# Kernel optimization log

Measured on AMD Instinct MI355X. Metric: run time of the kernel, lower is better.

The kernel has to match this reference:

```python
import jax, jax.numpy as jnp
import numpy as np

N, C_IN, HF, WF = 4, 256, 128, 128
IMG_H, IMG_W = 1024, 1024
A = 3  # anchors per location (1 size x 3 aspect ratios), matches RPNHead
OBJ_THR, IOU_THR = 0.3, 0.7
PRE_NMS, POST_NMS = 2000, 300  # pre-NMS top-k (== top_k_proposals_training), post-NMS top-k (testing)


def setup_inputs() -> dict:
    key = jax.random.key(0)
    ks = jax.random.split(key, 5)
    return {
        "feat": jax.random.normal(ks[0], (N, C_IN, HF, WF), jnp.float32),
        "conv_w": jax.random.normal(ks[1], (256, C_IN, 3, 3), jnp.float32) * 0.02,
        "conv_b": jnp.zeros((256,), jnp.float32),
        "det_w": jax.random.normal(ks[2], (A, 256, 1, 1), jnp.float32) * 0.05,
        "det_b": jnp.zeros((A,), jnp.float32),
        "reg_w": jax.random.normal(ks[3], (4 * A, 256, 1, 1), jnp.float32) * 0.02,
        "reg_b": jnp.zeros((4 * A,), jnp.float32),
    }


def _conv(x, w, b, pad):
    y = jax.lax.conv_general_dilated(x, w, (1, 1), [(pad, pad), (pad, pad)],
                                     dimension_numbers=("NCHW", "OIHW", "NCHW"))
    return y + b[None, :, None, None]


def _anchors():
    # AnchorGenerator.generate_anchors + grid_anchors, stride = image // grid
    scales = jnp.array([128.0], jnp.float32)
    ratios = jnp.array([0.5, 1.0, 2.0], jnp.float32)
    hr = jnp.sqrt(ratios)
    wr = 1.0 / hr
    ws = (wr[:, None] * scales[None, :]).reshape(-1)
    hs = (hr[:, None] * scales[None, :]).reshape(-1)
    base = jnp.round(jnp.stack([-ws, -hs, ws, hs], axis=1) / 2.0)  # [A,4]
    sx = jnp.arange(WF, dtype=jnp.float32) * (IMG_W // WF)
    sy = jnp.arange(HF, dtype=jnp.float32) * (IMG_H // HF)
    yy, xx = jnp.meshgrid(sy, sx, indexing="ij")
    shifts = jnp.stack([xx.ravel(), yy.ravel(), xx.ravel(), yy.ravel()], axis=1)  # [H*W,4]
    return (shifts[:, None, :] + base[None, :, :]).reshape(-1, 4)  # [H*W*A,4]


def _decode(anchors, deltas):
    # Faithful to source, including the x/y swap in the anchor-center computation.
    x1, y1, x2, y2 = anchors[..., 0], anchors[..., 1], anchors[..., 2], anchors[..., 3]
    aw = x2 - x1
    ah = y2 - y1
    acx = y1 + aw / 2  # (sic) matches original code
    acy = x1 + ah / 2  # (sic)
    dx, dy, dw, dh = deltas[..., 0], deltas[..., 1], deltas[..., 2], deltas[..., 3]
    px = acx + dx * aw
    py = acy + dy * ah
    pw = aw * jnp.exp(dw)
    ph = ah * jnp.exp(dh)
    return jnp.stack([px - pw / 2, py - ph / 2, px + pw / 2, py + ph / 2], axis=-1)


def _filter_one(boxes, scores):
    # clip -> degenerate filter -> objectness threshold -> NMS -> top-k, fixed shapes
    w = boxes[:, 2] - boxes[:, 0]
    h = boxes[:, 3] - boxes[:, 1]
    valid = (scores > OBJ_THR) & (w > 0) & (h > 0)
    s = jnp.where(valid, scores, -jnp.inf)
    top_s, top_i = jax.lax.top_k(s, PRE_NMS)
    b = boxes[top_i]
    v = valid[top_i]
    area = jnp.maximum(b[:, 2] - b[:, 0], 0) * jnp.maximum(b[:, 3] - b[:, 1], 0)
    ix1 = jnp.maximum(b[:, None, 0], b[None, :, 0])
    iy1 = jnp.maximum(b[:, None, 1], b[None, :, 1])
    ix2 = jnp.minimum(b[:, None, 2], b[None, :, 2])
    iy2 = jnp.minimum(b[:, None, 3], b[None, :, 3])
    inter = jnp.maximum(ix2 - ix1, 0) * jnp.maximum(iy2 - iy1, 0)
    iou = inter / jnp.maximum(area[:, None] + area[None, :] - inter, 1e-9)
    idxs = jnp.arange(PRE_NMS)

    def body(keep, i):
        sup = jnp.any((iou[i] > IOU_THR) & keep & (idxs < i))
        return keep.at[i].set(v[i] & ~sup), None

    keep, _ = jax.lax.scan(body, jnp.zeros(PRE_NMS, bool), idxs)
    fs = jnp.where(keep, top_s, -jnp.inf)
    sel_s, sel_i = jax.lax.top_k(fs, POST_NMS)
    kept = keep[sel_i]
    out = jnp.concatenate([b[sel_i], sel_s[:, None]], axis=-1)  # [POST,5] = box + score
    return jnp.where(kept[:, None], out, 0.0)


def reference(feat, conv_w, conv_b, det_w, det_b, reg_w, reg_b):
    x = _conv(feat, conv_w, conv_b, 1)                      # fpn conv 3x3, no activation
    obj = jax.nn.sigmoid(_conv(x, det_w, det_b, 0)).reshape(N, -1)  # [N, A*H*W]
    d = _conv(x, reg_w, reg_b, 0)                           # [N, 4A, H, W]
    d = d.reshape(N, 4, A, HF, WF).transpose(0, 2, 3, 4, 1).reshape(N, -1, 4)
    anchors = _anchors()                                    # [A_total, 4]
    props = _decode(anchors[None], d)
    props = jnp.stack([
        jnp.clip(props[..., 0], 0, IMG_W), jnp.clip(props[..., 1], 0, IMG_H),
        jnp.clip(props[..., 2], 0, IMG_W), jnp.clip(props[..., 3], 0, IMG_H)], axis=-1)
    return jax.vmap(_filter_one)(props, obj)  # [N, POST_NMS, 5]
```

## Files before the change

### kernel.cpp

```cpp
#include <hip/hip_runtime.h>
#include <hip/hip_bf16.h>
#include <hip/hip_fp16.h>
#include <stdint.h>
#include <math.h>

#define N_IMG 4
#define CIN 256
#define HFD 128
#define WFD 128
#define HW (HFD*WFD)
#define NA 3
#define NPROP (NA*HW)
#define PRE_NMS 2000
#define POST_NMS 300

__device__ __forceinline__ unsigned long long rl64(unsigned long long v, int i) {
    unsigned int lo = (unsigned int)__builtin_amdgcn_readlane((int)(unsigned int)v, i);
    unsigned int hi = (unsigned int)__builtin_amdgcn_readlane((int)(unsigned int)(v >> 32), i);
    return ((unsigned long long)hi << 32) | (unsigned long long)lo;
}

__device__ __forceinline__ double sum4(const double* __restrict__ PART, size_t cp) {
    const size_t S = (size_t)1 << 20;
    return (PART[cp] + PART[cp + S]) + (PART[cp + 2 * S] + PART[cp + 3 * S]);
}

__device__ __forceinline__ void decode_box(int i, double dx, double dy, double dwv, double dhv,
                                           double& c1o, double& c2o, double& c3o, double& c4o) {
    int loc = i / 3, aa = i % 3;
    int hh = loc >> 7, wwi = loc & 127;
    double sx = (double)(wwi * 8), sy = (double)(hh * 8);
    double bx1 = (aa == 0) ? -91.0 : (aa == 1 ? -64.0 : -45.0);
    double by1 = (aa == 0) ? -45.0 : (aa == 1 ? -64.0 : -91.0);
    double x1 = sx + bx1, y1 = sy + by1, x2 = sx - bx1, y2 = sy - by1;
    double aw = x2 - x1, ahh = y2 - y1;
    double acx = y1 + aw * 0.5;
    double acy = x1 + ahh * 0.5;
    double px = acx + dx * aw, py = acy + dy * ahh;
    double pw = aw * exp(dwv), ph = ahh * exp(dhv);
    double c1 = px - pw * 0.5, c2 = py - ph * 0.5, c3 = px + pw * 0.5, c4 = py + ph * 0.5;
    c1o = fmin(fmax(c1, 0.0), 1024.0);
    c2o = fmin(fmax(c2, 0.0), 1024.0);
    c3o = fmin(fmax(c3, 0.0), 1024.0);
    c4o = fmin(fmax(c4, 0.0), 1024.0);
}

__global__ __launch_bounds__(256) void k_effw64(const float* __restrict__ cw, const float* __restrict__ cb,
                                                const float* __restrict__ dw_, const float* __restrict__ db_,
                                                const float* __restrict__ rw_, const float* __restrict__ rb_,
                                                double* __restrict__ E64, double* __restrict__ EB64,
                                                unsigned long long* __restrict__ PSPREF,
                                                int* __restrict__ PSNEED,
                                                uint32_t* __restrict__ HIST,
                                                uint32_t* __restrict__ CNT)
{
    int b = blockIdx.x;
    int tid = threadIdx.x;
    if (b < 144) {
        __shared__ float hwl[15][260];
        __shared__ float wt[256][16];
        int k0 = b * 16;
        for (int idx = tid; idx < 15 * 256; idx += 256) {
            int c = idx >> 8, co = idx & 255;
            hwl[c][co] = (c < 3) ? dw_[c * 256 + co] : rw_[(c - 3) * 256 + co];
        }
        for (int idx = tid; idx < 4096; idx += 256) {
            int co = idx >> 4, kk = idx & 15;
            wt[co][kk] = cw[co * 2304 + k0 + kk];
        }
        __syncthreads();
        int kk = tid >> 4, c = tid & 15;
        double s = 0.0;
        if (c < 15) {
#pragma unroll 4
            for (int co = 0; co < 256; co++) s += (double)hwl[c][co] * (double)wt[co][kk];
        }
        E64[(k0 + kk) * 16 + c] = s;
    } else {
        if (tid < 16) {
            int c = tid;
            double s = 0.0; double hb = 0.0;
            if (c < 15) {
                const float* hw = (c < 3) ? (dw_ + c * 256) : (rw_ + (c - 3) * 256);
                for (int co = 0; co < 256; co++) s += (double)hw[co] * (double)cb[co];
                hb = (double)((c < 3) ? db_[c] : rb_[c - 3]);
            }
            EB64[c] = s + hb;
        }
        for (int i = tid; i < N_IMG * 2048; i += 256) HIST[i] = 0u;
        if (tid < N_IMG) { PSPREF[tid] = 0ull; PSNEED[tid] = PRE_NMS; CNT[tid] = 0u; }
    }
}

__global__ __launch_bounds__(256, 4) void k_conv64(const float* __restrict__ feat,
                                                   const double* __restrict__ E64,
                                                   double* __restrict__ PART)
{
    __shared__ float in_t[8][4][132];
    __shared__ double wl[8][9][16];
    int b = blockIdx.x;
    int chunk = b & 3; int hp = (b >> 2) & 63; int n = b >> 8;
    int h0 = hp * 2;
    int tid = threadIdx.x;
    int q = tid & 63;
    int row = q >> 5, qq = q & 31, w0 = qq * 4;
    int g = tid >> 6;
    double acc[4][4];
#pragma unroll
    for (int cc = 0; cc < 4; cc++)
#pragma unroll
        for (int px = 0; px < 4; px++) acc[cc][px] = 0.0;

    for (int sl = 0; sl < 8; sl++) {
        int ci0 = (chunk << 6) + sl * 8;
        for (int t = tid; t < 1024; t += 256) {
            int seg = t & 31;
            int rid = t >> 5;
            int ci = rid >> 2, dr = rid & 3;
            int gh = h0 - 1 + dr;
            float4 v = make_float4(0.f, 0.f, 0.f, 0.f);
            if (gh >= 0 && gh < HFD)
                v = *(const float4*)&feat[(((size_t)((n << 8) + ci0 + ci)) << 14) + (gh << 7) + (seg << 2)];
            float* d = &in_t[ci][dr][1 + (seg << 2)];
            d[0] = v.x; d[1] = v.y; d[2] = v.z; d[3] = v.w;
        }
        if (tid < 128) {
            int ci = tid >> 4, r2 = tid & 15, dr = r2 >> 2, col = r2 & 3;
            if (col < 3) in_t[ci][dr][col == 0 ? 0 : 128 + col] = 0.f;
        }
        for (int idx = tid; idx < 1152; idx += 256) {
            ((double*)wl)[idx] = E64[(size_t)ci0 * 144 + idx];
        }
        __syncthreads();
        for (int ci = 0; ci < 8; ci++) {
#pragma unroll
            for (int r = 0; r < 3; r++) {
                const float* rp = &in_t[ci][row + r][w0];
                float2 a0 = *(const float2*)(rp);
                float2 a1 = *(const float2*)(rp + 2);
                float2 a2 = *(const float2*)(rp + 4);
                double fv[6];
                fv[0] = (double)a0.x; fv[1] = (double)a0.y;
                fv[2] = (double)a1.x; fv[3] = (double)a1.y;
                fv[4] = (double)a2.x; fv[5] = (double)a2.y;
#pragma unroll
                for (int s = 0; s < 3; s++) {
                    const double* wp = &wl[ci][r * 3 + s][g * 4];
                    double2 wv0 = *(const double2*)(wp);
                    double2 wv1 = *(const double2*)(wp + 2);
#pragma unroll
                    for (int px = 0; px < 4; px++) {
                        double f = fv[s + px];
                        acc[0][px] += wv0.x * f;
                        acc[1][px] += wv0.y * f;
                        acc[2][px] += wv1.x * f;
                        acc[3][px] += wv1.y * f;
                    }
                }
            }
        }
        __syncthreads();
    }
    int gpos = (n << 14) + ((h0 + row) << 7) + w0;
    double* base = PART + ((size_t)chunk << 20) + gpos;
#pragma unroll
    for (int cc = 0; cc < 4; cc++) {
        int c = g * 4 + cc;
        if (c < 15) {
            double2 s0; s0.x = acc[cc][0]; s0.y = acc[cc][1];
            double2 s1; s1.x = acc[cc][2]; s1.y = acc[cc][3];
            *(double2*)(base + (size_t)c * 65536) = s0;
            *(double2*)(base + (size_t)c * 65536 + 2) = s1;
        }
    }
}

__global__ __launch_bounds__(256) void k_findecode(const double* __restrict__ PART,
                                                   const double* __restrict__ EB64,
                                                   unsigned long long* __restrict__ KEY64,
                                                   uint32_t* __restrict__ HIST)
{
    __shared__ uint32_t h2[2048];
    int tid = threadIdx.x;
    for (int i = tid; i < 2048; i += 256) h2[i] = 0u;
    __syncthreads();
    int p = blockIdx.x * 256 + tid;
    int n = p >> 14, pos = p & 16383;
    double L[15];
#pragma unroll
    for (int c = 0; c < 15; c++)
        L[c] = sum4(PART, (size_t)c * 65536 + p) + EB64[c];
#pragma unroll
    for (int a = 0; a < 3; a++) {
        double logit = L[a];
        double score = 1.0 / (1.0 + exp(-logit));
        int i = a * HW + pos;
        double c1, c2, c3, c4;
        decode_box(i, L[3 + a], L[6 + a], L[9 + a], L[12 + a], c1, c2, c3, c4);
        bool valid = (score > 0.3) && (c3 - c1 > 0.0) && (c4 - c2 > 0.0);
        unsigned long long key = valid ? ~((unsigned long long)__double_as_longlong(score)) : ~0ull;
        KEY64[(size_t)n * NPROP + i] = key;
        atomicAdd(&h2[(uint32_t)(key >> 53)], 1u);
    }
    __syncthreads();
    uint32_t* G = HIST + n * 2048;
    for (int i = tid; i < 2048; i += 256) {
        uint32_t v = h2[i];
        if (v) atomicAdd(&G[i], v);
    }
}

__global__ __launch_bounds__(256) void k_hist(const unsigned long long* __restrict__ KEY64,
                                              const unsigned long long* __restrict__ PSPREF,
                                              uint32_t* __restrict__ HIST, int L)
{
    __shared__ uint32_t h[2048];
    int blk = blockIdx.x; int n = blk >> 4, sub = blk & 15;
    int tid = threadIdx.x;
    for (int i = tid; i < 2048; i += 256) h[i] = 0u;
    __syncthreads();
    int sh = 53 - 11 * L;
    unsigned long long pref = PSPREF[n];
    const unsigned long long* K = KEY64 + (size_t)n * NPROP + sub * 3072;
    for (int i = tid; i < 3072; i += 256) {
        unsigned long long k = K[i];
        bool in = (L == 0) || ((k >> (sh + 11)) == pref);
        if (in) atomicAdd(&h[(uint32_t)((k >> sh) & 2047ull)], 1u);
    }
    __syncthreads();
    uint32_t* G = HIST + n * 2048;
    for (int i = tid; i < 2048; i += 256) {
        uint32_t v = h[i];
        if (v) atomicAdd(&G[i], v);
    }
}

__global__ __launch_bounds__(256) void k_pick(uint32_t* __restrict__ HIST,
                                              unsigned long long* __restrict__ PSPREF,
                                              int* __restrict__ PSNEED)
{
    int n = blockIdx.x; int tid = threadIdx.x;
    __shared__ uint32_t hl[2048];
    __shared__ uint32_t psum[256];
    uint32_t* G = HIST + n * 2048;
    for (int i = tid; i < 2048; i += 256) hl[i] = G[i];
    __syncthreads();
    {
        uint32_t s = 0;
        for (int qq = 0; qq < 8; qq++) s += hl[tid * 8 + qq];
        psum[tid] = s;
    }
    __syncthreads();
    if (tid == 0) {
        int need = PSNEED[n];
        unsigned long long pref = PSPREF[n];
        uint32_t cum = 0; int g = 255;
        for (int t = 0; t < 256; t++) { uint32_t c = psum[t]; if (cum + c >= (uint32_t)need) { g = t; break; } cum += c; }
        int bsel = g * 8 + 7;
        for (int t = g * 8; t < g * 8 + 8; t++) { uint32_t c = hl[t]; if (cum + c >= (uint32_t)need) { bsel = t; break; } cum += c; }
        PSNEED[n] = need - (int)cum;
        PSPREF[n] = (pref << 11) | (unsigned long long)bsel;
    }
    __syncthreads();
    for (int i = tid; i < 2048; i += 256) G[i] = 0u;
}

__global__ __launch_bounds__(256) void k_collect(const unsigned long long* __restrict__ KEY64,
                                                 const unsigned long long* __restrict__ PSPREF,
                                                 uint32_t* __restrict__ CNT,
                                                 unsigned long long* __restrict__ CANDK,
                                                 uint32_t* __restrict__ CANDI)
{
    int blk = blockIdx.x; int n = blk >> 4, sub = blk & 15;
    int tid = threadIdx.x;
    unsigned long long pref44 = PSPREF[n];
    const unsigned long long* K = KEY64 + (size_t)n * NPROP;
    int base = sub * 3072;
    for (int i = tid; i < 3072; i += 256) {
        unsigned long long k = K[base + i];
        if (k != ~0ull && (k >> 20) <= pref44) {
            uint32_t p2 = atomicAdd(&CNT[n], 1u);
            if (p2 < 2048u) { CANDK[n * 2048 + p2] = k; CANDI[n * 2048 + p2] = (uint32_t)(base + i); }
        }
    }
}

__global__ __launch_bounds__(1024) void k_finalsel(const uint32_t* __restrict__ CNT,
                                                   const unsigned long long* __restrict__ CANDK,
                                                   const uint32_t* __restrict__ CANDI,
                                                   const double* __restrict__ PART,
                                                   const double* __restrict__ EB64,
                                                   unsigned long long* __restrict__ skeys,
                                                   double* __restrict__ bsort,
                                                   double* __restrict__ area)
{
    int n = blockIdx.x; int tid = threadIdx.x;
    __shared__ unsigned long long selk[2048];
    __shared__ uint32_t seli[2048];
    uint32_t cnt = CNT[n]; if (cnt > 2048u) cnt = 2048u;
    for (int t = tid; t < 2048; t += 1024) {
        if (t < (int)cnt) { selk[t] = CANDK[n * 2048 + t]; seli[t] = CANDI[n * 2048 + t]; }
        else { selk[t] = ~0ull; seli[t] = 0xFFFFFFFFu; }
    }
    __syncthreads();
    for (unsigned k2 = 2; k2 <= 2048; k2 <<= 1) {
        for (unsigned jx = k2 >> 1; jx > 0; jx >>= 1) {
            for (int t = tid; t < 2048; t += 1024) {
                unsigned ixj = (unsigned)t ^ jx;
                if (ixj > (unsigned)t) {
                    bool up = ((t & k2) == 0);
                    unsigned long long ka = selk[t], kb = selk[ixj];
                    uint32_t ia = seli[t], ib = seli[ixj];
                    bool agt = (ka > kb) || (ka == kb && ia > ib);
                    if (up ? agt : !agt) {
                        selk[t] = kb; selk[ixj] = ka;
                        seli[t] = ib; seli[ixj] = ia;
                    }
                }
            }
            __syncthreads();
        }
    }
    for (int t = tid; t < 2048; t += 1024) {
        bool valid = (t < PRE_NMS) && (selk[t] != ~0ull);
        if (t < PRE_NMS) skeys[(size_t)n * PRE_NMS + t] = valid ? selk[t] : ~0ull;
        double b0 = 0, b1 = 0, b2 = 0, b3 = 0;
        if (valid) {
            int i = (int)seli[t];
            int a = i >> 14, pos = i & 16383;
            size_t p = ((size_t)n << 14) + pos;
            double dx  = sum4(PART, (size_t)(3 + a)  * 65536 + p) + EB64[3 + a];
            double dy  = sum4(PART, (size_t)(6 + a)  * 65536 + p) + EB64[6 + a];
            double dwv = sum4(PART, (size_t)(9 + a)  * 65536 + p) + EB64[9 + a];
            double dhv = sum4(PART, (size_t)(12 + a) * 65536 + p) + EB64[12 + a];
            decode_box(i, dx, dy, dwv, dhv, b0, b1, b2, b3);
        }
        double* bs = bsort + (((size_t)(n * 2048 + t)) << 2);
        bs[0] = b0; bs[1] = b1; bs[2] = b2; bs[3] = b3;
        area[(size_t)n * 2048 + t] = fmax(b2 - b0, 0.0) * fmax(b3 - b1, 0.0);
    }
}

__global__ __launch_bounds__(256) void k_iou2(const double* __restrict__ bsort,
                                              const double* __restrict__ area,
                                              unsigned long long* __restrict__ mat)
{
    int blk = blockIdx.x; int n = blk >> 6; int rt = blk & 63;
    int tid = threadIdx.x;
    int r = tid >> 3, g = tid & 7;
    int i = rt * 32 + r;
    const double* bp = bsort + ((size_t)n * 2048 + i) * 4;
    double bx0 = bp[0], bx1_ = bp[1], bx2_ = bp[2], bx3 = bp[3];
    double ai = area[(size_t)n * 2048 + i];
    __shared__ double cbx[512][4];
    __shared__ double ca[512];
    for (int cc = 0; cc < 4; cc++) {
        if ((cc + 1) * 512 <= rt * 32) continue;
        __syncthreads();
        for (int idx = tid; idx < 512; idx += 256) {
            const double* sp = bsort + ((size_t)n * 2048 + cc * 512 + idx) * 4;
            cbx[idx][0] = sp[0]; cbx[idx][1] = sp[1]; cbx[idx][2] = sp[2]; cbx[idx][3] = sp[3];
            ca[idx] = area[(size_t)n * 2048 + cc * 512 + idx];
        }
        __syncthreads();
        unsigned long long wd = 0ull;
        for (int jb = 0; jb < 64; jb++) {
            int jr = (jb + g * 9) & 63;
            int jj = g * 64 + jr;
            double ix1 = fmax(bx0, cbx[jj][0]);
            double iy1 = fmax(bx1_, cbx[jj][1]);
            double ix2 = fmin(bx2_, cbx[jj][2]);
            double iy2 = fmin(bx3, cbx[jj][3]);
            double inter = fmax(ix2 - ix1, 0.0) * fmax(iy2 - iy1, 0.0);
            double den = fmax(ai + ca[jj] - inter, 1e-9);
            double iou = inter / den;
            if (iou > 0.7) wd |= (1ull << jr);
        }
        mat[((size_t)n * 2048 + i) * 32 + cc * 8 + g] = wd;
    }
}

__global__ __launch_bounds__(256) void k_nms3(const unsigned long long* __restrict__ skeys,
                                              const double* __restrict__ bsort,
                                              const unsigned long long* __restrict__ mat,
                                              float* __restrict__ out)
{
    int n = blockIdx.x; int tid = threadIdx.x;
    int lane = tid & 63;
    __shared__ unsigned long long rb[2][64][33];
    __shared__ unsigned long long sup_lds[32];
    __shared__ unsigned long long vb[32];
    __shared__ unsigned long long kbw[32];
    __shared__ int s_stop;
    float* dout = out + n * (POST_NMS * 5);
    for (int t = tid; t < POST_NMS * 5; t += 256) dout[t] = 0.f;
    if (tid < 32) { sup_lds[tid] = 0ull; kbw[tid] = 0ull; }
    if (tid == 0) s_stop = 0;
    if (tid < 64) {
        for (int i0 = 0; i0 < 2048; i0 += 64) {
            int i = i0 + lane;
            unsigned long long k = (i < PRE_NMS) ? skeys[(size_t)n * PRE_NMS + i] : ~0ull;
            unsigned long long m = __ballot(k != ~0ull);
            if (lane == 0) vb[i0 >> 6] = m;
        }
    }
    int r = tid >> 2, w0 = (tid & 3) * 8;
    {
        const unsigned long long* src = mat + ((size_t)n * 2048 + r) * 32 + w0;
        ulonglong2 a = *(const ulonglong2*)(src);
        ulonglong2 b = *(const ulonglong2*)(src + 2);
        ulonglong2 c2 = *(const ulonglong2*)(src + 4);
        ulonglong2 d = *(const ulonglong2*)(src + 6);
        unsigned long long* dst = &rb[0][r][w0];
        dst[0] = a.x; dst[1] = a.y; dst[2] = b.x; dst[3] = b.y;
        dst[4] = c2.x; dst[5] = c2.y; dst[6] = d.x; dst[7] = d.y;
    }
    __syncthreads();
    int total_kept = 0;
    for (int c = 0; c < 32; c++) {
        if (s_stop) break;
        int cur = c & 1, nxt = cur ^ 1;
        ulonglong2 pa, pb, pc, pd;
        bool pf = (c + 1 < 32);
        if (pf) {
            const unsigned long long* src = mat + ((size_t)n * 2048 + (c + 1) * 64 + r) * 32 + w0;
            pa = *(const ulonglong2*)(src);
            pb = *(const ulonglong2*)(src + 2);
            pc = *(const ulonglong2*)(src + 4);
            pd = *(const ulonglong2*)(src + 6);
        }
        if (tid < 64) {
            unsigned long long M = rb[cur][lane][c];
            unsigned long long supw = sup_lds[c];
            unsigned long long vbw = vb[c];
            unsigned long long km = 0ull;
#pragma unroll
            for (int ii = 0; ii < 64; ii++) {
                unsigned long long bit = 1ull << ii;
                if ((vbw & bit) && !(supw & bit)) {
                    km |= bit;
                    supw |= rl64(M, ii);
                }
            }
            if (lane == 0) {
                kbw[c] = km;
                total_kept += __popcll(km);
                if (total_kept >= POST_NMS) s_stop = 1;
            }
        }
        __syncthreads();
        {
            int w = tid & 31, g = tid >> 5;
            unsigned long long km2 = kbw[c];
            unsigned long long sub = (km2 >> (g * 8)) & 0xFFull;
            unsigned long long acc = 0ull;
            while (sub) {
                int bpos = __ffsll((long long)sub) - 1;
                sub &= sub - 1;
                acc |= rb[cur][g * 8 + bpos][w];
            }
            if (acc) atomicOr(&sup_lds[w], acc);
        }
        if (pf) {
            unsigned long long* dst = &rb[nxt][r][w0];
            dst[0] = pa.x; dst[1] = pa.y; dst[2] = pb.x; dst[3] = pb.y;
            dst[4] = pc.x; dst[5] = pc.y; dst[6] = pd.x; dst[7] = pd.y;
        }
        __syncthreads();
    }
    if (tid < 64) {
        int running = 0;
        for (int i0 = 0; i0 < 2048; i0 += 64) {
            int i = i0 + lane;
            bool kp = (i < PRE_NMS) && ((kbw[i >> 6] >> (i & 63)) & 1ull);
            unsigned long long m = __ballot(kp);
            if (kp) {
                int rk = running + __popcll(m & ((1ull << lane) - 1ull));
                if (rk < POST_NMS) {
                    const double* bp2 = bsort + ((size_t)n * 2048 + i) * 4;
                    unsigned long long k = skeys[(size_t)n * PRE_NMS + i];
                    double s = __longlong_as_double((long long)~k);
                    float* o = dout + rk * 5;
                    o[0] = (float)bp2[0]; o[1] = (float)bp2[1];
                    o[2] = (float)bp2[2]; o[3] = (float)bp2[3];
                    o[4] = (float)s;
                }
            }
            running += __popcll(m);
        }
    }
}

extern "C" void kernel_launch(void* const* d_in, const int* in_sizes, int n_in,
                              void* d_out, int out_size, void* d_ws, size_t ws_size,
                              hipStream_t stream) {
    (void)in_sizes; (void)n_in; (void)out_size; (void)ws_size;
    const float* feat   = (const float*)d_in[0];
    const float* conv_w = (const float*)d_in[1];
    const float* conv_b = (const float*)d_in[2];
    const float* det_w  = (const float*)d_in[3];
    const float* det_b  = (const float*)d_in[4];
    const float* reg_w  = (const float*)d_in[5];
    const float* reg_b  = (const float*)d_in[6];
    float* out = (float*)d_out;

    char* w = (char*)d_ws;
    double* E64 = (double*)w;                          w += (size_t)2304 * 16 * 8;
    double* EB64 = (double*)w;                         w += 128;
    double* PART = (double*)w;                         w += (size_t)4 << 23;
    unsigned long long* KEY64 = (unsigned long long*)w; w += (size_t)N_IMG * NPROP * 8;
    unsigned long long* PSPREF = (unsigned long long*)w; w += N_IMG * 8;
    int* PSNEED = (int*)w;                             w += 64;
    uint32_t* HIST = (uint32_t*)w;                     w += (size_t)N_IMG * 2048 * 4;
    uint32_t* CNT = (uint32_t*)w;                      w += 64;
    unsigned long long* CANDK = (unsigned long long*)w; w += (size_t)N_IMG * 2048 * 8;
    uint32_t* CANDI = (uint32_t*)w;                    w += (size_t)N_IMG * 2048 * 4;
    unsigned long long* SKEY = (unsigned long long*)w; w += (size_t)N_IMG * PRE_NMS * 8;
    double* BSORT = (double*)w;                        w += (size_t)N_IMG * 2048 * 4 * 8;
    double* AREA = (double*)w;                         w += (size_t)N_IMG * 2048 * 8;
    unsigned long long* MAT = (unsigned long long*)w;  w += (size_t)N_IMG * 2048 * 32 * 8;

    k_effw64<<<dim3(145), dim3(256), 0, stream>>>(conv_w, conv_b, det_w, det_b, reg_w, reg_b,
                                                  E64, EB64, PSPREF, PSNEED, HIST, CNT);
    k_conv64<<<dim3(1024), dim3(256), 0, stream>>>(feat, E64, PART);
    k_findecode<<<dim3(256), dim3(256), 0, stream>>>(PART, EB64, KEY64, HIST);
    k_pick<<<dim3(N_IMG), dim3(256), 0, stream>>>(HIST, PSPREF, PSNEED);
    for (int L = 1; L < 4; L++) {
        k_hist<<<dim3(64), dim3(256), 0, stream>>>(KEY64, PSPREF, HIST, L);
        k_pick<<<dim3(N_IMG), dim3(256), 0, stream>>>(HIST, PSPREF, PSNEED);
    }
    k_collect<<<dim3(64), dim3(256), 0, stream>>>(KEY64, PSPREF, CNT, CANDK, CANDI);
    k_finalsel<<<dim3(N_IMG), dim3(1024), 0, stream>>>(CNT, CANDK, CANDI, PART, EB64, SKEY, BSORT, AREA);
    k_iou2<<<dim3(N_IMG * 64), dim3(256), 0, stream>>>(BSORT, AREA, MAT);
    k_nms3<<<dim3(N_IMG), dim3(256), 0, stream>>>(SKEY, BSORT, MAT, out);
}
```

Baseline: 374.5 us.

## Split conv channels across more threads and fold pick into last hist block

The head-conv kernel now runs 512 threads per block. Each thread accumulates 2 output channels instead of 4, which cuts registers per thread and is meant to raise occupancy, at the cost of reading and converting the input tile twice as often. The separate k_pick launches are removed: the last block to finish each histogram kernel, found through an atomic DONE counter and thread fences, performs the prefix pick for all images. This saves four small kernel launches and their serialization gaps, but adds a grid-wide completion pattern that depends on correct memory fencing.

```diff
diff --git a/kernel.cpp b/kernel.cpp
--- a/kernel.cpp
+++ b/kernel.cpp
@@ -45,6 +45,33 @@
     c4o = fmin(fmax(c4, 0.0), 1024.0);
 }
 
+__device__ __forceinline__ void pick_one(uint32_t* __restrict__ G,
+                                         unsigned long long* __restrict__ PSPREF,
+                                         int* __restrict__ PSNEED, int n,
+                                         int tid, uint32_t* hl, uint32_t* psum) {
+    for (int i = tid; i < 2048; i += 256) hl[i] = G[i];
+    __syncthreads();
+    if (tid < 256) {
+        uint32_t s = 0;
+        for (int qq = 0; qq < 8; qq++) s += hl[tid * 8 + qq];
+        psum[tid] = s;
+    }
+    __syncthreads();
+    if (tid == 0) {
+        int need = PSNEED[n];
+        unsigned long long pref = PSPREF[n];
+        uint32_t cum = 0; int g = 255;
+        for (int t = 0; t < 256; t++) { uint32_t c = psum[t]; if (cum + c >= (uint32_t)need) { g = t; break; } cum += c; }
+        int bsel = g * 8 + 7;
+        for (int t = g * 8; t < g * 8 + 8; t++) { uint32_t c = hl[t]; if (cum + c >= (uint32_t)need) { bsel = t; break; } cum += c; }
+        PSNEED[n] = need - (int)cum;
+        PSPREF[n] = (pref << 11) | (unsigned long long)bsel;
+    }
+    __syncthreads();
+    for (int i = tid; i < 2048; i += 256) G[i] = 0u;
+    __syncthreads();
+}
+
 __global__ __launch_bounds__(256) void k_effw64(const float* __restrict__ cw, const float* __restrict__ cb,
                                                 const float* __restrict__ dw_, const float* __restrict__ db_,
                                                 const float* __restrict__ rw_, const float* __restrict__ rb_,
@@ -52,7 +79,8 @@
                                                 unsigned long long* __restrict__ PSPREF,
                                                 int* __restrict__ PSNEED,
                                                 uint32_t* __restrict__ HIST,
-                                                uint32_t* __restrict__ CNT)
+                                                uint32_t* __restrict__ CNT,
+                                                uint32_t* __restrict__ DONE)
 {
     int b = blockIdx.x;
     int tid = threadIdx.x;
@@ -89,10 +117,11 @@
         }
         for (int i = tid; i < N_IMG * 2048; i += 256) HIST[i] = 0u;
         if (tid < N_IMG) { PSPREF[tid] = 0ull; PSNEED[tid] = PRE_NMS; CNT[tid] = 0u; }
-    }
-}
-
-__global__ __launch_bounds__(256, 4) void k_conv64(const float* __restrict__ feat,
+        if (tid < 8) DONE[tid] = 0u;
+    }
+}
+
+__global__ __launch_bounds__(512, 8) void k_conv64(const float* __restrict__ feat,
                                                    const double* __restrict__ E64,
                                                    double* __restrict__ PART)
 {
@@ -105,15 +134,15 @@
     int q = tid & 63;
     int row = q >> 5, qq = q & 31, w0 = qq * 4;
     int g = tid >> 6;
-    double acc[4][4];
-#pragma unroll
-    for (int cc = 0; cc < 4; cc++)
+    double acc[2][4];
+#pragma unroll
+    for (int cc = 0; cc < 2; cc++)
 #pragma unroll
         for (int px = 0; px < 4; px++) acc[cc][px] = 0.0;
 
     for (int sl = 0; sl < 8; sl++) {
         int ci0 = (chunk << 6) + sl * 8;
-        for (int t = tid; t < 1024; t += 256) {
+        for (int t = tid; t < 1024; t += 512) {
             int seg = t & 31;
             int rid = t >> 5;
             int ci = rid >> 2, dr = rid & 3;
@@ -128,7 +157,7 @@
             int ci = tid >> 4, r2 = tid & 15, dr = r2 >> 2, col = r2 & 3;
             if (col < 3) in_t[ci][dr][col == 0 ? 0 : 128 + col] = 0.f;
         }
-        for (int idx = tid; idx < 1152; idx += 256) {
+        for (int idx = tid; idx < 1152; idx += 512) {
             ((double*)wl)[idx] = E64[(size_t)ci0 * 144 + idx];
         }
         __syncthreads();
@@ -145,16 +174,12 @@
                 fv[4] = (double)a2.x; fv[5] = (double)a2.y;
 #pragma unroll
                 for (int s = 0; s < 3; s++) {
-                    const double* wp = &wl[ci][r * 3 + s][g * 4];
-                    double2 wv0 = *(const double2*)(wp);
-                    double2 wv1 = *(const double2*)(wp + 2);
+                    const double2 wv = *(const double2*)&wl[ci][r * 3 + s][g * 2];
 #pragma unroll
                     for (int px = 0; px < 4; px++) {
                         double f = fv[s + px];
-                        acc[0][px] += wv0.x * f;
-                        acc[1][px] += wv0.y * f;
-                        acc[2][px] += wv1.x * f;
-                        acc[3][px] += wv1.y * f;
+                        acc[0][px] += wv.x * f;
+                        acc[1][px] += wv.y * f;
                     }
                 }
             }
@@ -164,8 +189,8 @@
     int gpos = (n << 14) + ((h0 + row) << 7) + w0;
     double* base = PART + ((size_t)chunk << 20) + gpos;
 #pragma unroll
-    for (int cc = 0; cc < 4; cc++) {
-        int c = g * 4 + cc;
+    for (int cc = 0; cc < 2; cc++) {
+        int c = g * 2 + cc;
         if (c < 15) {
             double2 s0; s0.x = acc[cc][0]; s0.y = acc[cc][1];
             double2 s1; s1.x = acc[cc][2]; s1.y = acc[cc][3];
@@ -178,9 +203,14 @@
 __global__ __launch_bounds__(256) void k_findecode(const double* __restrict__ PART,
                                                    const double* __restrict__ EB64,
                                                    unsigned long long* __restrict__ KEY64,
-                                                   uint32_t* __restrict__ HIST)
+                                                   uint32_t* __restrict__ HIST,
+                                                   uint32_t* __restrict__ DONE,
+                                                   unsigned long long* __restrict__ PSPREF,
+                                                   int* __restrict__ PSNEED)
 {
     __shared__ uint32_t h2[2048];
+    __shared__ uint32_t psum[256];
+    __shared__ uint32_t s_rank;
     int tid = threadIdx.x;
     for (int i = tid; i < 2048; i += 256) h2[i] = 0u;
     __syncthreads();
@@ -208,13 +238,25 @@
         uint32_t v = h2[i];
         if (v) atomicAdd(&G[i], v);
     }
-}
-
-__global__ __launch_bounds__(256) void k_hist(const unsigned long long* __restrict__ KEY64,
-                                              const unsigned long long* __restrict__ PSPREF,
-                                              uint32_t* __restrict__ HIST, int L)
+    __threadfence();
+    if (tid == 0) s_rank = atomicAdd(&DONE[0], 1u);
+    __syncthreads();
+    if (s_rank == 255u) {
+        __threadfence();
+        for (int n2 = 0; n2 < N_IMG; n2++)
+            pick_one(HIST + n2 * 2048, PSPREF, PSNEED, n2, tid, h2, psum);
+    }
+}
+
+__global__ __launch_bounds__(256) void k_histpick(const unsigned long long* __restrict__ KEY64,
+                                                  unsigned long long* __restrict__ PSPREF,
+                                                  int* __restrict__ PSNEED,
+                                                  uint32_t* __restrict__ HIST,
+                                                  uint32_t* __restrict__ DONE, int L)
 {
     __shared__ uint32_t h[2048];
+    __shared__ uint32_t psum[256];
+    __shared__ uint32_t s_rank;
     int blk = blockIdx.x; int n = blk >> 4, sub = blk & 15;
     int tid = threadIdx.x;
     for (int i = tid; i < 2048; i += 256) h[i] = 0u;
@@ -224,8 +266,7 @@
     const unsigned long long* K = KEY64 + (size_t)n * NPROP + sub * 3072;
     for (int i = tid; i < 3072; i += 256) {
         unsigned long long k = K[i];
-        bool in = (L == 0) || ((k >> (sh + 11)) == pref);
-        if (in) atomicAdd(&h[(uint32_t)((k >> sh) & 2047ull)], 1u);
+        if ((k >> (sh + 11)) == pref) atomicAdd(&h[(uint32_t)((k >> sh) & 2047ull)], 1u);
     }
     __syncthreads();
     uint32_t* G = HIST + n * 2048;
@@ -233,36 +274,14 @@
         uint32_t v = h[i];
         if (v) atomicAdd(&G[i], v);
     }
-}
-
-__global__ __launch_bounds__(256) void k_pick(uint32_t* __restrict__ HIST,
-                                              unsigned long long* __restrict__ PSPREF,
-                                              int* __restrict__ PSNEED)
-{
-    int n = blockIdx.x; int tid = threadIdx.x;
-    __shared__ uint32_t hl[2048];
-    __shared__ uint32_t psum[256];
-    uint32_t* G = HIST + n * 2048;
-    for (int i = tid; i < 2048; i += 256) hl[i] = G[i];
-    __syncthreads();
-    {
-        uint32_t s = 0;
-        for (int qq = 0; qq < 8; qq++) s += hl[tid * 8 + qq];
-        psum[tid] = s;
-    }
-    __syncthreads();
-    if (tid == 0) {
-        int need = PSNEED[n];
-        unsigned long long pref = PSPREF[n];
-        uint32_t cum = 0; int g = 255;
-        for (int t = 0; t < 256; t++) { uint32_t c = psum[t]; if (cum + c >= (uint32_t)need) { g = t; break; } cum += c; }
-        int bsel = g * 8 + 7;
-        for (int t = g * 8; t < g * 8 + 8; t++) { uint32_t c = hl[t]; if (cum + c >= (uint32_t)need) { bsel = t; break; } cum += c; }
-        PSNEED[n] = need - (int)cum;
-        PSPREF[n] = (pref << 11) | (unsigned long long)bsel;
-    }
-    __syncthreads();
-    for (int i = tid; i < 2048; i += 256) G[i] = 0u;
+    __threadfence();
+    if (tid == 0) s_rank = atomicAdd(&DONE[L], 1u);
+    __syncthreads();
+    if (s_rank == 63u) {
+        __threadfence();
+        for (int n2 = 0; n2 < N_IMG; n2++)
+            pick_one(HIST + n2 * 2048, PSPREF, PSNEED, n2, tid, h, psum);
+    }
 }
 
 __global__ __launch_bounds__(256) void k_collect(const unsigned long long* __restrict__ KEY64,
@@ -513,6 +532,7 @@
     int* PSNEED = (int*)w;                             w += 64;
     uint32_t* HIST = (uint32_t*)w;                     w += (size_t)N_IMG * 2048 * 4;
     uint32_t* CNT = (uint32_t*)w;                      w += 64;
+    uint32_t* DONE = (uint32_t*)w;                     w += 64;
     unsigned long long* CANDK = (unsigned long long*)w; w += (size_t)N_IMG * 2048 * 8;
     uint32_t* CANDI = (uint32_t*)w;                    w += (size_t)N_IMG * 2048 * 4;
     unsigned long long* SKEY = (unsigned long long*)w; w += (size_t)N_IMG * PRE_NMS * 8;
@@ -521,13 +541,11 @@
     unsigned long long* MAT = (unsigned long long*)w;  w += (size_t)N_IMG * 2048 * 32 * 8;
 
     k_effw64<<<dim3(145), dim3(256), 0, stream>>>(conv_w, conv_b, det_w, det_b, reg_w, reg_b,
-                                                  E64, EB64, PSPREF, PSNEED, HIST, CNT);
-    k_conv64<<<dim3(1024), dim3(256), 0, stream>>>(feat, E64, PART);
-    k_findecode<<<dim3(256), dim3(256), 0, stream>>>(PART, EB64, KEY64, HIST);
-    k_pick<<<dim3(N_IMG), dim3(256), 0, stream>>>(HIST, PSPREF, PSNEED);
+                                                  E64, EB64, PSPREF, PSNEED, HIST, CNT, DONE);
+    k_conv64<<<dim3(1024), dim3(512), 0, stream>>>(feat, E64, PART);
+    k_findecode<<<dim3(256), dim3(256), 0, stream>>>(PART, EB64, KEY64, HIST, DONE, PSPREF, PSNEED);
     for (int L = 1; L < 4; L++) {
-        k_hist<<<dim3(64), dim3(256), 0, stream>>>(KEY64, PSPREF, HIST, L);
-        k_pick<<<dim3(N_IMG), dim3(256), 0, stream>>>(HIST, PSPREF, PSNEED);
+        k_histpick<<<dim3(64), dim3(256), 0, stream>>>(KEY64, PSPREF, PSNEED, HIST, DONE, L);
     }
     k_collect<<<dim3(64), dim3(256), 0, stream>>>(KEY64, PSPREF, CNT, CANDK, CANDI);
     k_finalsel<<<dim3(N_IMG), dim3(1024), 0, stream>>>(CNT, CANDK, CANDI, PART, EB64, SKEY, BSORT, AREA);
```

New measurement: 488.7 us. 30.5% more time.
